# Kernel optimization log

Measured on AMD Instinct MI355X. Metric: run time of the kernel, lower is better.

Reference implementation:

```python
import jax, jax.numpy as jnp
import numpy as np

B, N, P, HID = 1024, 30, 16, 128
NR = N * (N - 1)          # 870 directed edges
DR, DE, DO, NT = 3, 5, 6, 5


def _lin(x, w, b):
    return x @ w.T + b


def setup_inputs() -> dict:
    key = jax.random.key(0)
    ks = jax.random.split(key, 24)

    def w(k, o, i):
        return jax.random.normal(k, (o, i), jnp.float32) * 0.05

    def bias(k, o):
        return jax.random.normal(k, (o,), jnp.float32) * 0.05

    return {
        "x": jax.random.normal(ks[0], (B, N, P), jnp.float32),
        "RR": jax.random.normal(ks[1], (B, N, NR), jnp.float32),
        "RS": jax.random.normal(ks[2], (B, N, NR), jnp.float32),
        "RA": jax.random.normal(ks[3], (B, DR, NR), jnp.float32),
        "fr1_w": w(ks[4], HID, 2 * P + DR), "fr1_b": bias(ks[5], HID),
        "fr2_w": w(ks[6], HID // 2, HID),   "fr2_b": bias(ks[7], HID // 2),
        "fr3_w": w(ks[8], DE, HID // 2),    "fr3_b": bias(ks[9], DE),
        "fo1_w": w(ks[10], HID, P + DE),    "fo1_b": bias(ks[11], HID),
        "fo2_w": w(ks[12], HID // 2, HID),  "fo2_b": bias(ks[13], HID // 2),
        "fo3_w": w(ks[14], DO, HID // 2),   "fo3_b": bias(ks[15], DO),
        "fc1_w": w(ks[16], HID, DO * N),    "fc1_b": bias(ks[17], HID),
        "fc2_w": w(ks[18], HID // 2, HID),  "fc2_b": bias(ks[19], HID // 2),
        "fc3_w": w(ks[20], NT, HID // 2),   "fc3_b": bias(ks[21], NT),
    }


def reference(x, RR, RS, RA,
              fr1_w, fr1_b, fr2_w, fr2_b, fr3_w, fr3_b,
              fo1_w, fo1_b, fo2_w, fo2_b, fo3_w, fo3_b,
              fc1_w, fc1_b, fc2_w, fc2_b, fc3_w, fc3_b):
    xt = jnp.swapaxes(x, 1, 2)                       # [B, P, N]
    Orr = jnp.einsum('bpn,bnr->bpr', xt, RR)          # [B, P, Nr]
    Ors = jnp.einsum('bpn,bnr->bpr', xt, RS)          # [B, P, Nr]
    Bm = jnp.concatenate([Orr, Ors, RA], axis=1)      # [B, 2P+Dr, Nr]
    Bm = jnp.swapaxes(Bm, 1, 2)                       # [B, Nr, 2P+Dr]
    h = jax.nn.relu(_lin(Bm, fr1_w, fr1_b))
    h = jax.nn.relu(_lin(h, fr2_w, fr2_b))
    E = jax.nn.relu(_lin(h, fr3_w, fr3_b))            # [B, Nr, De]
    Ebar = jnp.einsum('bre,bnr->ben', E, RR)          # E^T @ RR^T -> [B, De, N]
    C = jnp.concatenate([xt, Ebar], axis=1)           # [B, P+De, N]
    C = jnp.swapaxes(C, 1, 2)                         # [B, N, P+De]
    h = jax.nn.relu(_lin(C, fo1_w, fo1_b))
    h = jax.nn.relu(_lin(h, fo2_w, fo2_b))
    O = jax.nn.relu(_lin(h, fo3_w, fo3_b))            # [B, N, Do]
    f = O.reshape(O.shape[0], -1)                     # [B, Do*N]
    f = jax.nn.relu(_lin(f, fc1_w, fc1_b))
    f = jax.nn.relu(_lin(f, fc2_w, fc2_b))
    return _lin(f, fc3_w, fc3_b)                      # [B, n_targets]
```

## Files before the change

kernel.cpp:

```cpp
#include <hip/hip_runtime.h>

#define B_ 1024
#define N_ 30
#define P_ 16
#define NR_ 870
#define DR_ 3
#define DE_ 5
#define DO_ 6
#define NT_ 5

typedef unsigned short ushort_t;
typedef __attribute__((ext_vector_type(8))) short short8_t;
typedef __attribute__((ext_vector_type(4))) float f32x4;

union Frag { short8_t v; ushort_t u[8]; };

__device__ __forceinline__ float bf2f(ushort_t u) {
    union { unsigned int i; float f; } v; v.i = ((unsigned int)u) << 16; return v.f;
}
__device__ __forceinline__ ushort_t f2bf(float f) {
    union { float f; unsigned int i; } v; v.f = f;
    unsigned int x = v.i;
    return (ushort_t)((x + 0x7FFFu + ((x >> 16) & 1u)) >> 16);
}
__device__ __forceinline__ void split(float v, ushort_t& h, ushort_t& l) {
    h = f2bf(v);
    float r = v - bf2f(h);
    l = f2bf(r);
}
__device__ __forceinline__ f32x4 mfma(short8_t a, short8_t b, f32x4 c) {
    return __builtin_amdgcn_mfma_f32_16x16x32_bf16(a, b, c, 0, 0, 0);
}

__global__ __launch_bounds__(256) void k_prep(
    const float* __restrict__ x,  const float* __restrict__ w1,
    const float* __restrict__ w2, const float* __restrict__ wo1,
    const float* __restrict__ wo2,
    ushort_t* __restrict__ xAh,  ushort_t* __restrict__ xAl,
    ushort_t* __restrict__ w1h,  ushort_t* __restrict__ w1l,
    ushort_t* __restrict__ w2h,  ushort_t* __restrict__ w2l,
    ushort_t* __restrict__ wo1h, ushort_t* __restrict__ wo1l,
    ushort_t* __restrict__ wo2h, ushort_t* __restrict__ wo2l)
{
    const int blk = blockIdx.x, tid = threadIdx.x;
    if (blk < 1024) {
        int b = blk;
        for (int idx = tid; idx < 512; idx += 256) {
            int lane = idx >> 3, j = idx & 7;
            int p = lane & 15, n = (lane >> 4) * 8 + j;
            float v = (n < N_) ? x[(b * N_ + n) * P_ + p] : 0.f;
            ushort_t h_, l_; split(v, h_, l_);
            xAh[b * 512 + idx] = h_; xAl[b * 512 + idx] = l_;
        }
    } else if (blk == 1024) {
        for (int idx = tid; idx < 16 * 512; idx += 256) {
            int f = idx >> 9, eps = idx & 511;
            int lane = eps >> 3, j = eps & 7;
            int mt = f >> 1, kt = f & 1;
            int m = mt * 16 + (lane & 15);
            int k = kt * 32 + (lane >> 4) * 8 + j;
            float v = (k < 35) ? w1[m * 35 + k] : 0.f;
            ushort_t h_, l_; split(v, h_, l_);
            w1h[idx] = h_; w1l[idx] = l_;
        }
    } else if (blk == 1025) {
        for (int idx = tid; idx < 16 * 512; idx += 256) {
            int f = idx >> 9, eps = idx & 511;
            int lane = eps >> 3, j = eps & 7;
            int mt = f >> 2, kt = f & 3;
            int m = mt * 16 + (lane & 15);
            int k = kt * 32 + (lane >> 4) * 8 + j;
            float v = w2[m * 128 + k];
            ushort_t h_, l_; split(v, h_, l_);
            w2h[idx] = h_; w2l[idx] = l_;
        }
    } else if (blk == 1026) {
        for (int idx = tid; idx < 8 * 512; idx += 256) {
            int f = idx >> 9, eps = idx & 511;
            int lane = eps >> 3, j = eps & 7;
            int m = f * 16 + (lane & 15);
            int k = (lane >> 4) * 8 + j;
            float v = (k < 21) ? wo1[m * 21 + k] : 0.f;
            ushort_t h_, l_; split(v, h_, l_);
            wo1h[idx] = h_; wo1l[idx] = l_;
        }
    } else {
        for (int idx = tid; idx < 16 * 512; idx += 256) {
            int f = idx >> 9, eps = idx & 511;
            int lane = eps >> 3, j = eps & 7;
            int mt = f >> 2, kt = f & 3;
            int m = mt * 16 + (lane & 15);
            int k = kt * 32 + (lane >> 4) * 8 + j;
            float v = wo2[m * 128 + k];
            ushort_t h_, l_; split(v, h_, l_);
            wo2h[idx] = h_; wo2l[idx] = l_;
        }
    }
}

__global__ __launch_bounds__(256) void k_edge(
    const float* __restrict__ RR, const float* __restrict__ RS,
    const float* __restrict__ RA,
    const float* __restrict__ b1, const float* __restrict__ b2,
    const float* __restrict__ w3, const float* __restrict__ b3,
    const ushort_t* __restrict__ xAh, const ushort_t* __restrict__ xAl,
    const ushort_t* __restrict__ w1h, const ushort_t* __restrict__ w1l,
    const ushort_t* __restrict__ w2h, const ushort_t* __restrict__ w2l,
    float* __restrict__ Ebar)
{
    const int b   = blockIdx.y;
    const int r0  = blockIdx.x * 64;
    const int tid = threadIdx.x;
    const int lane = tid & 63;
    const int wv   = tid >> 6;
    const int l15  = lane & 15;
    const int q    = lane >> 4;

    __shared__ union {
        ushort_t aT[2][64][72];
        float    h2T[64][68];
    } u1;
    __shared__ union {
        ushort_t h1T[2][64][72];
        float    rs[30][70];
    } u2;
    __shared__ float rrs[30][70];
    __shared__ float Ee[64][6];
    __shared__ float b1s[128], b2s[64];

    if (tid < 128) b1s[tid] = b1[tid];
    if (tid < 64)  b2s[tid] = b2[tid];

    for (int idx = tid; idx < 30 * 32; idx += 256) {
        int n = idx >> 5, g = idx & 31;
        int r = r0 + 2 * g;
        const float* pr = &RR[(b * N_ + n) * NR_];
        const float* ps = &RS[(b * N_ + n) * NR_];
        float v0, v1, s0, s1;
        if (r + 1 < NR_) {
            float2 a = *(const float2*)&pr[r]; v0 = a.x; v1 = a.y;
            float2 c = *(const float2*)&ps[r]; s0 = c.x; s1 = c.y;
        } else {
            int ra_ = r < NR_ ? r : NR_ - 1;
            int rb_ = (r + 1) < NR_ ? (r + 1) : NR_ - 1;
            v0 = pr[ra_]; v1 = pr[rb_]; s0 = ps[ra_]; s1 = ps[rb_];
        }
        rrs[n][2 * g] = v0;  rrs[n][2 * g + 1] = v1;
        u2.rs[n][2 * g] = s0; u2.rs[n][2 * g + 1] = s1;
    }
    __syncthreads();

    const int eloc = wv * 16 + l15;
    const int r = r0 + eloc;
    const bool rvalid = (r < NR_);

    {
        Frag xh, xl;
        xh.v = ((const short8_t*)xAh)[b * 64 + lane];
        xl.v = ((const short8_t*)xAl)[b * 64 + lane];

        Frag rrh, rrl, rsh, rsl;
        #pragma unroll
        for (int j = 0; j < 8; ++j) {
            int n = q * 8 + j;
            float vr = 0.f, vs = 0.f;
            if (n < N_) { vr = rrs[n][eloc]; vs = u2.rs[n][eloc]; }
            ushort_t h_, l_;
            split(vr, h_, l_); rrh.u[j] = h_; rrl.u[j] = l_;
            split(vs, h_, l_); rsh.u[j] = h_; rsl.u[j] = l_;
        }

        f32x4 aR = {0.f,0.f,0.f,0.f}, aS = {0.f,0.f,0.f,0.f};
        aR = mfma(xh.v, rrh.v, aR); aR = mfma(xl.v, rrh.v, aR); aR = mfma(xh.v, rrl.v, aR);
        aS = mfma(xh.v, rsh.v, aS); aS = mfma(xl.v, rsh.v, aS); aS = mfma(xh.v, rsl.v, aS);

        uint4 z = {0u,0u,0u,0u};
        *(uint4*)&u1.aT[0][eloc][32 + q * 8] = z;
        *(uint4*)&u1.aT[1][eloc][32 + q * 8] = z;

        ushort4 ph, pl; ushort_t h_, l_;
        split(aR[0], h_, l_); ph.x = h_; pl.x = l_;
        split(aR[1], h_, l_); ph.y = h_; pl.y = l_;
        split(aR[2], h_, l_); ph.z = h_; pl.z = l_;
        split(aR[3], h_, l_); ph.w = h_; pl.w = l_;
        *(ushort4*)&u1.aT[0][eloc][q * 4] = ph;
        *(ushort4*)&u1.aT[1][eloc][q * 4] = pl;
        split(aS[0], h_, l_); ph.x = h_; pl.x = l_;
        split(aS[1], h_, l_); ph.y = h_; pl.y = l_;
        split(aS[2], h_, l_); ph.z = h_; pl.z = l_;
        split(aS[3], h_, l_); ph.w = h_; pl.w = l_;
        *(ushort4*)&u1.aT[0][eloc][16 + q * 4] = ph;
        *(ushort4*)&u1.aT[1][eloc][16 + q * 4] = pl;

        if (q < DR_) {
            float v = rvalid ? RA[(b * DR_ + q) * NR_ + r] : 0.f;
            split(v, h_, l_);
            u1.aT[0][eloc][32 + q] = h_;
            u1.aT[1][eloc][32 + q] = l_;
        }
    }
    __syncthreads();

    short8_t W2hf[4], W2lf[4];
    #pragma unroll
    for (int kt = 0; kt < 4; ++kt) {
        W2hf[kt] = ((const short8_t*)w2h)[(wv * 4 + kt) * 64 + lane];
        W2lf[kt] = ((const short8_t*)w2l)[(wv * 4 + kt) * 64 + lane];
    }
    f32x4 acc2[4];
    #pragma unroll
    for (int et = 0; et < 4; ++et) acc2[et] = (f32x4){0.f,0.f,0.f,0.f};

    #pragma unroll
    for (int hf = 0; hf < 2; ++hf) {
        {
            const int mt = hf * 4 + wv;
            short8_t W1hf_[2], W1lf_[2];
            #pragma unroll
            for (int kt = 0; kt < 2; ++kt) {
                W1hf_[kt] = ((const short8_t*)w1h)[(mt * 2 + kt) * 64 + lane];
                W1lf_[kt] = ((const short8_t*)w1l)[(mt * 2 + kt) * 64 + lane];
            }
            #pragma unroll
            for (int et = 0; et < 4; ++et) {
                int e = et * 16 + l15;
                f32x4 acc = {0.f,0.f,0.f,0.f};
                #pragma unroll
                for (int kt = 0; kt < 2; ++kt) {
                    short8_t Bh = *(const short8_t*)&u1.aT[0][e][kt * 32 + q * 8];
                    short8_t Bl = *(const short8_t*)&u1.aT[1][e][kt * 32 + q * 8];
                    acc = mfma(W1hf_[kt], Bh, acc);
                    acc = mfma(W1lf_[kt], Bh, acc);
                    acc = mfma(W1hf_[kt], Bl, acc);
                }
                ushort4 ph, pl; ushort_t h_, l_; float hv;
                hv = fmaxf(acc[0] + b1s[mt * 16 + q * 4 + 0], 0.f); split(hv, h_, l_); ph.x = h_; pl.x = l_;
                hv = fmaxf(acc[1] + b1s[mt * 16 + q * 4 + 1], 0.f); split(hv, h_, l_); ph.y = h_; pl.y = l_;
                hv = fmaxf(acc[2] + b1s[mt * 16 + q * 4 + 2], 0.f); split(hv, h_, l_); ph.z = h_; pl.z = l_;
                hv = fmaxf(acc[3] + b1s[mt * 16 + q * 4 + 3], 0.f); split(hv, h_, l_); ph.w = h_; pl.w = l_;
                *(ushort4*)&u2.h1T[0][e][wv * 16 + q * 4] = ph;
                *(ushort4*)&u2.h1T[1][e][wv * 16 + q * 4] = pl;
            }
        }
        __syncthreads();

        #pragma unroll
        for (int et = 0; et < 4; ++et) {
            int e = et * 16 + l15;
            #pragma unroll
            for (int ktl = 0; ktl < 2; ++ktl) {
                short8_t bh = *(const short8_t*)&u2.h1T[0][e][ktl * 32 + q * 8];
                short8_t bl = *(const short8_t*)&u2.h1T[1][e][ktl * 32 + q * 8];
                acc2[et] = mfma(W2hf[hf * 2 + ktl], bh, acc2[et]);
                acc2[et] = mfma(W2lf[hf * 2 + ktl], bh, acc2[et]);
                acc2[et] = mfma(W2hf[hf * 2 + ktl], bl, acc2[et]);
            }
        }
        if (hf == 1) {
            #pragma unroll
            for (int et = 0; et < 4; ++et) {
                int e = et * 16 + l15;
                float4 st;
                st.x = fmaxf(acc2[et][0] + b2s[wv * 16 + q * 4 + 0], 0.f);
                st.y = fmaxf(acc2[et][1] + b2s[wv * 16 + q * 4 + 1], 0.f);
                st.z = fmaxf(acc2[et][2] + b2s[wv * 16 + q * 4 + 2], 0.f);
                st.w = fmaxf(acc2[et][3] + b2s[wv * 16 + q * 4 + 3], 0.f);
                *(float4*)&u1.h2T[e][wv * 16 + q * 4] = st;
            }
        }
        __syncthreads();
    }

    for (int it = tid; it < 64 * DE_; it += 256) {
        int e = it / DE_, i = it - e * DE_;
        float s = b3[i];
        const float* wr = w3 + i * 64;
        #pragma unroll
        for (int k = 0; k < 64; k += 4) {
            float4 hv = *(const float4*)&u1.h2T[e][k];
            float4 wv4 = *(const float4*)&wr[k];
            s += hv.x * wv4.x + hv.y * wv4.y + hv.z * wv4.z + hv.w * wv4.w;
        }
        Ee[e][i] = ((r0 + e) < NR_) ? fmaxf(s, 0.f) : 0.f;
    }
    __syncthreads();

    if (tid < DE_ * N_) {
        int i = tid / N_, n = tid - i * N_;
        float s = 0.f;
        #pragma unroll
        for (int e = 0; e < 64; ++e) s += Ee[e][i] * rrs[n][e];
        atomicAdd(&Ebar[(b * DE_ + i) * N_ + n], s);
    }
}

__global__ __launch_bounds__(256) void k_node(
    const float* __restrict__ x, const float* __restrict__ Ebar,
    const float* __restrict__ bo1, const float* __restrict__ bo2,
    const float* __restrict__ wo3, const float* __restrict__ bo3,
    const ushort_t* __restrict__ wo1h, const ushort_t* __restrict__ wo1l,
    const ushort_t* __restrict__ wo2h, const ushort_t* __restrict__ wo2l,
    float* __restrict__ f180)
{
    const int b0 = blockIdx.x * 2;
    const int tid = threadIdx.x;
    const int lane = tid & 63;
    const int wv = tid >> 6;
    const int l15 = lane & 15;
    const int q = lane >> 4;

    __shared__ ushort_t cT[2][64][40];
    __shared__ ushort_t h1T[2][64][136];
    __shared__ float h2T[64][68];
    __shared__ float b1s[128], b2s[64];

    if (tid < 128) b1s[tid] = bo1[tid];
    if (tid < 64)  b2s[tid] = bo2[tid];

    for (int idx = tid; idx < 64 * 32; idx += 256) {
        int c = idx >> 5, k = idx & 31;
        int bb = c >> 5, n = c & 31;
        float v = 0.f;
        if (n < N_) {
            if (k < 16)      v = x[((b0 + bb) * N_ + n) * P_ + k];
            else if (k < 21) v = Ebar[((b0 + bb) * DE_ + (k - 16)) * N_ + n];
        }
        ushort_t h_, l_; split(v, h_, l_);
        cT[0][c][k] = h_; cT[1][c][k] = l_;
    }
    __syncthreads();

    {
        short8_t Wh[2], Wl[2];
        #pragma unroll
        for (int mi = 0; mi < 2; ++mi) {
            int mt = wv + mi * 4;
            Wh[mi] = ((const short8_t*)wo1h)[mt * 64 + lane];
            Wl[mi] = ((const short8_t*)wo1l)[mt * 64 + lane];
        }
        #pragma unroll
        for (int et = 0; et < 4; ++et) {
            int c = et * 16 + l15;
            short8_t bh = *(const short8_t*)&cT[0][c][q * 8];
            short8_t bl = *(const short8_t*)&cT[1][c][q * 8];
            #pragma unroll
            for (int mi = 0; mi < 2; ++mi) {
                int mt = wv + mi * 4;
                f32x4 acc = {0.f,0.f,0.f,0.f};
                acc = mfma(Wh[mi], bh, acc);
                acc = mfma(Wl[mi], bh, acc);
                acc = mfma(Wh[mi], bl, acc);
                ushort4 ph, pl; ushort_t h_, l_; float hv;
                hv = fmaxf(acc[0] + b1s[mt * 16 + q * 4 + 0], 0.f); split(hv, h_, l_); ph.x = h_; pl.x = l_;
                hv = fmaxf(acc[1] + b1s[mt * 16 + q * 4 + 1], 0.f); split(hv, h_, l_); ph.y = h_; pl.y = l_;
                hv = fmaxf(acc[2] + b1s[mt * 16 + q * 4 + 2], 0.f); split(hv, h_, l_); ph.z = h_; pl.z = l_;
                hv = fmaxf(acc[3] + b1s[mt * 16 + q * 4 + 3], 0.f); split(hv, h_, l_); ph.w = h_; pl.w = l_;
                *(ushort4*)&h1T[0][c][mt * 16 + q * 4] = ph;
                *(ushort4*)&h1T[1][c][mt * 16 + q * 4] = pl;
            }
        }
    }
    __syncthreads();

    {
        short8_t Wh[4], Wl[4];
        #pragma unroll
        for (int kt = 0; kt < 4; ++kt) {
            Wh[kt] = ((const short8_t*)wo2h)[(wv * 4 + kt) * 64 + lane];
            Wl[kt] = ((const short8_t*)wo2l)[(wv * 4 + kt) * 64 + lane];
        }
        #pragma unroll
        for (int et = 0; et < 4; ++et) {
            int c = et * 16 + l15;
            f32x4 acc = {0.f,0.f,0.f,0.f};
            #pragma unroll
            for (int kt = 0; kt < 4; ++kt) {
                short8_t bh = *(const short8_t*)&h1T[0][c][kt * 32 + q * 8];
                short8_t bl = *(const short8_t*)&h1T[1][c][kt * 32 + q * 8];
                acc = mfma(Wh[kt], bh, acc);
                acc = mfma(Wl[kt], bh, acc);
                acc = mfma(Wh[kt], bl, acc);
            }
            float4 st;
            st.x = fmaxf(acc[0] + b2s[wv * 16 + q * 4 + 0], 0.f);
            st.y = fmaxf(acc[1] + b2s[wv * 16 + q * 4 + 1], 0.f);
            st.z = fmaxf(acc[2] + b2s[wv * 16 + q * 4 + 2], 0.f);
            st.w = fmaxf(acc[3] + b2s[wv * 16 + q * 4 + 3], 0.f);
            *(float4*)&h2T[c][wv * 16 + q * 4] = st;
        }
    }
    __syncthreads();

    for (int it = tid; it < 384; it += 256) {
        int c = it / DO_, i = it - c * DO_;
        if (c < 64) {
            int bb = c >> 5, n = c & 31;
            if (n < N_) {
                float s = bo3[i];
                const float* wr = wo3 + i * 64;
                #pragma unroll
                for (int k = 0; k < 64; k += 4) {
                    float4 hv = *(const float4*)&h2T[c][k];
                    float4 wv4 = *(const float4*)&wr[k];
                    s += hv.x * wv4.x + hv.y * wv4.y + hv.z * wv4.z + hv.w * wv4.w;
                }
                f180[(b0 + bb) * 180 + n * DO_ + i] = fmaxf(s, 0.f);
            }
        }
    }
}

__global__ __launch_bounds__(256) void k_final(
    const float* __restrict__ f180,
    const float* __restrict__ wc1, const float* __restrict__ bc1,
    const float* __restrict__ wc2, const float* __restrict__ bc2,
    const float* __restrict__ wc3, const float* __restrict__ bc3,
    float* __restrict__ out)
{
    const int b0 = blockIdx.x * 2, tid = threadIdx.x;
    __shared__ float fs[2][184];
    __shared__ float h1s[2][128];
    __shared__ float h2s[2][64];

    for (int i = tid; i < 2 * 180; i += 256)
        fs[i / 180][i % 180] = f180[(b0 + i / 180) * 180 + (i % 180)];
    __syncthreads();

    {
        int bl = tid >> 7, j = tid & 127;
        const float* wr = wc1 + j * 180;
        float s = bc1[j];
        #pragma unroll 5
        for (int k = 0; k < 180; k += 4) {
            float4 wv = *(const float4*)&wr[k];
            s += fs[bl][k] * wv.x + fs[bl][k + 1] * wv.y
               + fs[bl][k + 2] * wv.z + fs[bl][k + 3] * wv.w;
        }
        h1s[bl][j] = fmaxf(s, 0.f);
    }
    __syncthreads();

    if (tid < 128) {
        int bl = tid >> 6, j = tid & 63;
        const float* wr = wc2 + j * 128;
        float s = bc2[j];
        #pragma unroll 4
        for (int k = 0; k < 128; k += 4) {
            float4 wv = *(const float4*)&wr[k];
            s += h1s[bl][k] * wv.x + h1s[bl][k + 1] * wv.y
               + h1s[bl][k + 2] * wv.z + h1s[bl][k + 3] * wv.w;
        }
        h2s[bl][j] = fmaxf(s, 0.f);
    }
    __syncthreads();

    if (tid < 10) {
        int bl = tid / 5, t = tid - bl * 5;
        const float* wr = wc3 + t * 64;
        float s = bc3[t];
        #pragma unroll
        for (int k = 0; k < 64; k += 4) {
            float4 wv = *(const float4*)&wr[k];
            s += h2s[bl][k] * wv.x + h2s[bl][k + 1] * wv.y
               + h2s[bl][k + 2] * wv.z + h2s[bl][k + 3] * wv.w;
        }
        out[(b0 + bl) * NT_ + t] = s;
    }
}

extern "C" void kernel_launch(void* const* d_in, const int* in_sizes, int n_in,
                              void* d_out, int out_size, void* d_ws, size_t ws_size,
                              hipStream_t stream)
{
    const float* x    = (const float*)d_in[0];
    const float* RR   = (const float*)d_in[1];
    const float* RS   = (const float*)d_in[2];
    const float* RA   = (const float*)d_in[3];
    const float* fr1w = (const float*)d_in[4];
    const float* fr1b = (const float*)d_in[5];
    const float* fr2w = (const float*)d_in[6];
    const float* fr2b = (const float*)d_in[7];
    const float* fr3w = (const float*)d_in[8];
    const float* fr3b = (const float*)d_in[9];
    const float* fo1w = (const float*)d_in[10];
    const float* fo1b = (const float*)d_in[11];
    const float* fo2w = (const float*)d_in[12];
    const float* fo2b = (const float*)d_in[13];
    const float* fo3w = (const float*)d_in[14];
    const float* fo3b = (const float*)d_in[15];
    const float* fc1w = (const float*)d_in[16];
    const float* fc1b = (const float*)d_in[17];
    const float* fc2w = (const float*)d_in[18];
    const float* fc2b = (const float*)d_in[19];
    const float* fc3w = (const float*)d_in[20];
    const float* fc3b = (const float*)d_in[21];
    float* out = (float*)d_out;

    float* Ebar = (float*)d_ws;
    float* f180 = Ebar + B_ * DE_ * N_;
    ushort_t* base = (ushort_t*)(f180 + B_ * 180);
    ushort_t* xAh  = base;             ushort_t* xAl  = xAh  + 1024 * 512;
    ushort_t* w1h  = xAl  + 1024*512;  ushort_t* w1l  = w1h  + 16 * 512;
    ushort_t* w2h  = w1l  + 16*512;    ushort_t* w2l  = w2h  + 16 * 512;
    ushort_t* wo1h = w2l  + 16*512;    ushort_t* wo1l = wo1h + 8 * 512;
    ushort_t* wo2h = wo1l + 8*512;     ushort_t* wo2l = wo2h + 16 * 512;

    hipMemsetAsync(Ebar, 0, (size_t)B_ * DE_ * N_ * sizeof(float), stream);

    k_prep<<<1028, 256, 0, stream>>>(x, fr1w, fr2w, fo1w, fo2w,
                                     xAh, xAl, w1h, w1l, w2h, w2l,
                                     wo1h, wo1l, wo2h, wo2l);

    dim3 g1(14, B_);
    k_edge<<<g1, 256, 0, stream>>>(RR, RS, RA, fr1b, fr2b, fr3w, fr3b,
                                   xAh, xAl, w1h, w1l, w2h, w2l, Ebar);
    k_node<<<B_ / 2, 256, 0, stream>>>(x, Ebar, fo1b, fo2b, fo3w, fo3b,
                                       wo1h, wo1l, wo2h, wo2l, f180);
    k_final<<<B_ / 2, 256, 0, stream>>>(f180, fc1w, fc1b, fc2w, fc2b,
                                        fc3w, fc3b, out);
}
```

Measured before the change: 632.0 us.

## Fuse node and final MLPs, load RR/RS directly, use packed bf16 conversion

```diff
diff --git a/kernel.cpp b/kernel.cpp
--- a/kernel.cpp
+++ b/kernel.cpp
@@ -13,7 +13,7 @@
 typedef __attribute__((ext_vector_type(8))) short short8_t;
 typedef __attribute__((ext_vector_type(4))) float f32x4;
 
-union Frag { short8_t v; ushort_t u[8]; };
+union Frag { short8_t v; ushort_t u[8]; unsigned int d[4]; };
 
 __device__ __forceinline__ float bf2f(ushort_t u) {
     union { unsigned int i; float f; } v; v.i = ((unsigned int)u) << 16; return v.f;
@@ -27,6 +27,18 @@
     h = f2bf(v);
     float r = v - bf2f(h);
     l = f2bf(r);
+}
+__device__ __forceinline__ unsigned int cvtpk(float a, float b) {
+    unsigned int r;
+    asm("v_cvt_pk_bf16_f32 %0, %1, %2" : "=v"(r) : "v"(a), "v"(b));
+    return r;
+}
+__device__ __forceinline__ void split2(float a, float b,
+                                       unsigned int& h, unsigned int& l) {
+    h = cvtpk(a, b);
+    union { unsigned int i; float f; } x0, x1;
+    x0.i = h << 16; x1.i = h & 0xFFFF0000u;
+    l = cvtpk(a - x0.f, b - x1.f);
 }
 __device__ __forceinline__ f32x4 mfma(short8_t a, short8_t b, f32x4 c) {
     return __builtin_amdgcn_mfma_f32_16x16x32_bf16(a, b, c, 0, 0, 0);
@@ -120,54 +132,35 @@
         ushort_t aT[2][64][72];
         float    h2T[64][68];
     } u1;
-    __shared__ union {
-        ushort_t h1T[2][64][72];
-        float    rs[30][70];
-    } u2;
-    __shared__ float rrs[30][70];
+    __shared__ ushort_t h1T[2][64][72];
     __shared__ float Ee[64][6];
     __shared__ float b1s[128], b2s[64];
 
     if (tid < 128) b1s[tid] = b1[tid];
     if (tid < 64)  b2s[tid] = b2[tid];
-
-    for (int idx = tid; idx < 30 * 32; idx += 256) {
-        int n = idx >> 5, g = idx & 31;
-        int r = r0 + 2 * g;
-        const float* pr = &RR[(b * N_ + n) * NR_];
-        const float* ps = &RS[(b * N_ + n) * NR_];
-        float v0, v1, s0, s1;
-        if (r + 1 < NR_) {
-            float2 a = *(const float2*)&pr[r]; v0 = a.x; v1 = a.y;
-            float2 c = *(const float2*)&ps[r]; s0 = c.x; s1 = c.y;
-        } else {
-            int ra_ = r < NR_ ? r : NR_ - 1;
-            int rb_ = (r + 1) < NR_ ? (r + 1) : NR_ - 1;
-            v0 = pr[ra_]; v1 = pr[rb_]; s0 = ps[ra_]; s1 = ps[rb_];
-        }
-        rrs[n][2 * g] = v0;  rrs[n][2 * g + 1] = v1;
-        u2.rs[n][2 * g] = s0; u2.rs[n][2 * g + 1] = s1;
-    }
-    __syncthreads();
 
     const int eloc = wv * 16 + l15;
     const int r = r0 + eloc;
     const bool rvalid = (r < NR_);
+    const int rc = rvalid ? r : NR_ - 1;
 
     {
         Frag xh, xl;
         xh.v = ((const short8_t*)xAh)[b * 64 + lane];
         xl.v = ((const short8_t*)xAl)[b * 64 + lane];
 
-        Frag rrh, rrl, rsh, rsl;
+        float vr[8], vs[8];
         #pragma unroll
         for (int j = 0; j < 8; ++j) {
             int n = q * 8 + j;
-            float vr = 0.f, vs = 0.f;
-            if (n < N_) { vr = rrs[n][eloc]; vs = u2.rs[n][eloc]; }
-            ushort_t h_, l_;
-            split(vr, h_, l_); rrh.u[j] = h_; rrl.u[j] = l_;
-            split(vs, h_, l_); rsh.u[j] = h_; rsl.u[j] = l_;
+            vr[j] = (n < N_) ? RR[(b * N_ + n) * NR_ + rc] : 0.f;
+            vs[j] = (n < N_) ? RS[(b * N_ + n) * NR_ + rc] : 0.f;
+        }
+        Frag rrh, rrl, rsh, rsl;
+        #pragma unroll
+        for (int d0 = 0; d0 < 4; ++d0) {
+            split2(vr[2*d0], vr[2*d0+1], rrh.d[d0], rrl.d[d0]);
+            split2(vs[2*d0], vs[2*d0+1], rsh.d[d0], rsl.d[d0]);
         }
 
         f32x4 aR = {0.f,0.f,0.f,0.f}, aS = {0.f,0.f,0.f,0.f};
@@ -178,23 +171,19 @@
         *(uint4*)&u1.aT[0][eloc][32 + q * 8] = z;
         *(uint4*)&u1.aT[1][eloc][32 + q * 8] = z;
 
-        ushort4 ph, pl; ushort_t h_, l_;
-        split(aR[0], h_, l_); ph.x = h_; pl.x = l_;
-        split(aR[1], h_, l_); ph.y = h_; pl.y = l_;
-        split(aR[2], h_, l_); ph.z = h_; pl.z = l_;
-        split(aR[3], h_, l_); ph.w = h_; pl.w = l_;
-        *(ushort4*)&u1.aT[0][eloc][q * 4] = ph;
-        *(ushort4*)&u1.aT[1][eloc][q * 4] = pl;
-        split(aS[0], h_, l_); ph.x = h_; pl.x = l_;
-        split(aS[1], h_, l_); ph.y = h_; pl.y = l_;
-        split(aS[2], h_, l_); ph.z = h_; pl.z = l_;
-        split(aS[3], h_, l_); ph.w = h_; pl.w = l_;
-        *(ushort4*)&u1.aT[0][eloc][16 + q * 4] = ph;
-        *(ushort4*)&u1.aT[1][eloc][16 + q * 4] = pl;
+        unsigned int h01, h23, l01, l23;
+        split2(aR[0], aR[1], h01, l01); split2(aR[2], aR[3], h23, l23);
+        { uint2 hh = {h01, h23}, ll = {l01, l23};
+          *(uint2*)&u1.aT[0][eloc][q * 4] = hh;
+          *(uint2*)&u1.aT[1][eloc][q * 4] = ll; }
+        split2(aS[0], aS[1], h01, l01); split2(aS[2], aS[3], h23, l23);
+        { uint2 hh = {h01, h23}, ll = {l01, l23};
+          *(uint2*)&u1.aT[0][eloc][16 + q * 4] = hh;
+          *(uint2*)&u1.aT[1][eloc][16 + q * 4] = ll; }
 
         if (q < DR_) {
             float v = rvalid ? RA[(b * DR_ + q) * NR_ + r] : 0.f;
-            split(v, h_, l_);
+            ushort_t h_, l_; split(v, h_, l_);
             u1.aT[0][eloc][32 + q] = h_;
             u1.aT[1][eloc][32 + q] = l_;
         }
@@ -233,13 +222,15 @@
                     acc = mfma(W1lf_[kt], Bh, acc);
                     acc = mfma(W1hf_[kt], Bl, acc);
                 }
-                ushort4 ph, pl; ushort_t h_, l_; float hv;
-                hv = fmaxf(acc[0] + b1s[mt * 16 + q * 4 + 0], 0.f); split(hv, h_, l_); ph.x = h_; pl.x = l_;
-                hv = fmaxf(acc[1] + b1s[mt * 16 + q * 4 + 1], 0.f); split(hv, h_, l_); ph.y = h_; pl.y = l_;
-                hv = fmaxf(acc[2] + b1s[mt * 16 + q * 4 + 2], 0.f); split(hv, h_, l_); ph.z = h_; pl.z = l_;
-                hv = fmaxf(acc[3] + b1s[mt * 16 + q * 4 + 3], 0.f); split(hv, h_, l_); ph.w = h_; pl.w = l_;
-                *(ushort4*)&u2.h1T[0][e][wv * 16 + q * 4] = ph;
-                *(ushort4*)&u2.h1T[1][e][wv * 16 + q * 4] = pl;
+                float hv0 = fmaxf(acc[0] + b1s[mt * 16 + q * 4 + 0], 0.f);
+                float hv1 = fmaxf(acc[1] + b1s[mt * 16 + q * 4 + 1], 0.f);
+                float hv2 = fmaxf(acc[2] + b1s[mt * 16 + q * 4 + 2], 0.f);
+                float hv3 = fmaxf(acc[3] + b1s[mt * 16 + q * 4 + 3], 0.f);
+                unsigned int d01, d23, e01, e23;
+                split2(hv0, hv1, d01, e01); split2(hv2, hv3, d23, e23);
+                uint2 hh = {d01, d23}, ll = {e01, e23};
+                *(uint2*)&h1T[0][e][wv * 16 + q * 4] = hh;
+                *(uint2*)&h1T[1][e][wv * 16 + q * 4] = ll;
             }
         }
         __syncthreads();
@@ -249,8 +240,8 @@
             int e = et * 16 + l15;
             #pragma unroll
             for (int ktl = 0; ktl < 2; ++ktl) {
-                short8_t bh = *(const short8_t*)&u2.h1T[0][e][ktl * 32 + q * 8];
-                short8_t bl = *(const short8_t*)&u2.h1T[1][e][ktl * 32 + q * 8];
+                short8_t bh = *(const short8_t*)&h1T[0][e][ktl * 32 + q * 8];
+                short8_t bl = *(const short8_t*)&h1T[1][e][ktl * 32 + q * 8];
                 acc2[et] = mfma(W2hf[hf * 2 + ktl], bh, acc2[et]);
                 acc2[et] = mfma(W2lf[hf * 2 + ktl], bh, acc2[et]);
                 acc2[et] = mfma(W2hf[hf * 2 + ktl], bl, acc2[et]);
@@ -287,20 +278,24 @@
 
     if (tid < DE_ * N_) {
         int i = tid / N_, n = tid - i * N_;
+        const float* pr = &RR[(b * N_ + n) * NR_ + r0];
+        const int emax = (NR_ - r0 < 64) ? (NR_ - r0) : 64;
         float s = 0.f;
-        #pragma unroll
-        for (int e = 0; e < 64; ++e) s += Ee[e][i] * rrs[n][e];
+        for (int e = 0; e < emax; ++e) s += Ee[e][i] * pr[e];
         atomicAdd(&Ebar[(b * DE_ + i) * N_ + n], s);
     }
 }
 
-__global__ __launch_bounds__(256) void k_node(
+__global__ __launch_bounds__(256) void k_nodef(
     const float* __restrict__ x, const float* __restrict__ Ebar,
     const float* __restrict__ bo1, const float* __restrict__ bo2,
     const float* __restrict__ wo3, const float* __restrict__ bo3,
     const ushort_t* __restrict__ wo1h, const ushort_t* __restrict__ wo1l,
     const ushort_t* __restrict__ wo2h, const ushort_t* __restrict__ wo2l,
-    float* __restrict__ f180)
+    const float* __restrict__ wc1, const float* __restrict__ bc1,
+    const float* __restrict__ wc2, const float* __restrict__ bc2,
+    const float* __restrict__ wc3, const float* __restrict__ bc3,
+    float* __restrict__ out)
 {
     const int b0 = blockIdx.x * 2;
     const int tid = threadIdx.x;
@@ -309,7 +304,10 @@
     const int l15 = lane & 15;
     const int q = lane >> 4;
 
-    __shared__ ushort_t cT[2][64][40];
+    __shared__ union {
+        ushort_t cT[2][64][40];
+        struct { float fs[2][184]; float h1s[2][128]; float h2s[2][64]; } f;
+    } u2n;
     __shared__ ushort_t h1T[2][64][136];
     __shared__ float h2T[64][68];
     __shared__ float b1s[128], b2s[64];
@@ -326,7 +324,7 @@
             else if (k < 21) v = Ebar[((b0 + bb) * DE_ + (k - 16)) * N_ + n];
         }
         ushort_t h_, l_; split(v, h_, l_);
-        cT[0][c][k] = h_; cT[1][c][k] = l_;
+        u2n.cT[0][c][k] = h_; u2n.cT[1][c][k] = l_;
     }
     __syncthreads();
 
@@ -341,8 +339,8 @@
         #pragma unroll
         for (int et = 0; et < 4; ++et) {
             int c = et * 16 + l15;
-            short8_t bh = *(const short8_t*)&cT[0][c][q * 8];
-            short8_t bl = *(const short8_t*)&cT[1][c][q * 8];
+            short8_t bh = *(const short8_t*)&u2n.cT[0][c][q * 8];
+            short8_t bl = *(const short8_t*)&u2n.cT[1][c][q * 8];
             #pragma unroll
             for (int mi = 0; mi < 2; ++mi) {
                 int mt = wv + mi * 4;
@@ -350,13 +348,15 @@
                 acc = mfma(Wh[mi], bh, acc);
                 acc = mfma(Wl[mi], bh, acc);
                 acc = mfma(Wh[mi], bl, acc);
-                ushort4 ph, pl; ushort_t h_, l_; float hv;
-                hv = fmaxf(acc[0] + b1s[mt * 16 + q * 4 + 0], 0.f); split(hv, h_, l_); ph.x = h_; pl.x = l_;
-                hv = fmaxf(acc[1] + b1s[mt * 16 + q * 4 + 1], 0.f); split(hv, h_, l_); ph.y = h_; pl.y = l_;
-                hv = fmaxf(acc[2] + b1s[mt * 16 + q * 4 + 2], 0.f); split(hv, h_, l_); ph.z = h_; pl.z = l_;
-                hv = fmaxf(acc[3] + b1s[mt * 16 + q * 4 + 3], 0.f); split(hv, h_, l_); ph.w = h_; pl.w = l_;
-                *(ushort4*)&h1T[0][c][mt * 16 + q * 4] = ph;
-                *(ushort4*)&h1T[1][c][mt * 16 + q * 4] = pl;
+                float hv0 = fmaxf(acc[0] + b1s[mt * 16 + q * 4 + 0], 0.f);
+                float hv1 = fmaxf(acc[1] + b1s[mt * 16 + q * 4 + 1], 0.f);
+                float hv2 = fmaxf(acc[2] + b1s[mt * 16 + q * 4 + 2], 0.f);
+                float hv3 = fmaxf(acc[3] + b1s[mt * 16 + q * 4 + 3], 0.f);
+                unsigned int d01, d23, e01, e23;
+                split2(hv0, hv1, d01, e01); split2(hv2, hv3, d23, e23);
+                uint2 hh = {d01, d23}, ll = {e01, e23};
+                *(uint2*)&h1T[0][c][mt * 16 + q * 4] = hh;
+                *(uint2*)&h1T[1][c][mt * 16 + q * 4] = ll;
             }
         }
     }
@@ -404,26 +404,10 @@
                     float4 wv4 = *(const float4*)&wr[k];
                     s += hv.x * wv4.x + hv.y * wv4.y + hv.z * wv4.z + hv.w * wv4.w;
                 }
-                f180[(b0 + bb) * 180 + n * DO_ + i] = fmaxf(s, 0.f);
-            }
-        }
-    }
-}
-
-__global__ __launch_bounds__(256) void k_final(
-    const float* __restrict__ f180,
-    const float* __restrict__ wc1, const float* __restrict__ bc1,
-    const float* __restrict__ wc2, const float* __restrict__ bc2,
-    const float* __restrict__ wc3, const float* __restrict__ bc3,
-    float* __restrict__ out)
-{
-    const int b0 = blockIdx.x * 2, tid = threadIdx.x;
-    __shared__ float fs[2][184];
-    __shared__ float h1s[2][128];
-    __shared__ float h2s[2][64];
-
-    for (int i = tid; i < 2 * 180; i += 256)
-        fs[i / 180][i % 180] = f180[(b0 + i / 180) * 180 + (i % 180)];
+                u2n.f.fs[bb][n * DO_ + i] = fmaxf(s, 0.f);
+            }
+        }
+    }
     __syncthreads();
 
     {
@@ -432,11 +416,11 @@
         float s = bc1[j];
         #pragma unroll 5
         for (int k = 0; k < 180; k += 4) {
-            float4 wv = *(const float4*)&wr[k];
-            s += fs[bl][k] * wv.x + fs[bl][k + 1] * wv.y
-               + fs[bl][k + 2] * wv.z + fs[bl][k + 3] * wv.w;
-        }
-        h1s[bl][j] = fmaxf(s, 0.f);
+            float4 wv4 = *(const float4*)&wr[k];
+            s += u2n.f.fs[bl][k] * wv4.x + u2n.f.fs[bl][k + 1] * wv4.y
+               + u2n.f.fs[bl][k + 2] * wv4.z + u2n.f.fs[bl][k + 3] * wv4.w;
+        }
+        u2n.f.h1s[bl][j] = fmaxf(s, 0.f);
     }
     __syncthreads();
 
@@ -446,11 +430,11 @@
         float s = bc2[j];
         #pragma unroll 4
         for (int k = 0; k < 128; k += 4) {
-            float4 wv = *(const float4*)&wr[k];
-            s += h1s[bl][k] * wv.x + h1s[bl][k + 1] * wv.y
-               + h1s[bl][k + 2] * wv.z + h1s[bl][k + 3] * wv.w;
-        }
-        h2s[bl][j] = fmaxf(s, 0.f);
+            float4 wv4 = *(const float4*)&wr[k];
+            s += u2n.f.h1s[bl][k] * wv4.x + u2n.f.h1s[bl][k + 1] * wv4.y
+               + u2n.f.h1s[bl][k + 2] * wv4.z + u2n.f.h1s[bl][k + 3] * wv4.w;
+        }
+        u2n.f.h2s[bl][j] = fmaxf(s, 0.f);
     }
     __syncthreads();
 
@@ -460,9 +444,9 @@
         float s = bc3[t];
         #pragma unroll
         for (int k = 0; k < 64; k += 4) {
-            float4 wv = *(const float4*)&wr[k];
-            s += h2s[bl][k] * wv.x + h2s[bl][k + 1] * wv.y
-               + h2s[bl][k + 2] * wv.z + h2s[bl][k + 3] * wv.w;
+            float4 wv4 = *(const float4*)&wr[k];
+            s += u2n.f.h2s[bl][k] * wv4.x + u2n.f.h2s[bl][k + 1] * wv4.y
+               + u2n.f.h2s[bl][k + 2] * wv4.z + u2n.f.h2s[bl][k + 3] * wv4.w;
         }
         out[(b0 + bl) * NT_ + t] = s;
     }
@@ -497,8 +481,7 @@
     float* out = (float*)d_out;
 
     float* Ebar = (float*)d_ws;
-    float* f180 = Ebar + B_ * DE_ * N_;
-    ushort_t* base = (ushort_t*)(f180 + B_ * 180);
+    ushort_t* base = (ushort_t*)(Ebar + B_ * DE_ * N_);
     ushort_t* xAh  = base;             ushort_t* xAl  = xAh  + 1024 * 512;
     ushort_t* w1h  = xAl  + 1024*512;  ushort_t* w1l  = w1h  + 16 * 512;
     ushort_t* w2h  = w1l  + 16*512;    ushort_t* w2l  = w2h  + 16 * 512;
@@ -514,8 +497,7 @@
     dim3 g1(14, B_);
     k_edge<<<g1, 256, 0, stream>>>(RR, RS, RA, fr1b, fr2b, fr3w, fr3b,
                                    xAh, xAl, w1h, w1l, w2h, w2l, Ebar);
-    k_node<<<B_ / 2, 256, 0, stream>>>(x, Ebar, fo1b, fo2b, fo3w, fo3b,
-                                       wo1h, wo1l, wo2h, wo2l, f180);
-    k_final<<<B_ / 2, 256, 0, stream>>>(f180, fc1w, fc1b, fc2w, fc2b,
-                                        fc3w, fc3b, out);
-}
+    k_nodef<<<B_ / 2, 256, 0, stream>>>(x, Ebar, fo1b, fo2b, fo3w, fo3b,
+                                        wo1h, wo1l, wo2h, wo2l,
+                                        fc1w, fc1b, fc2w, fc2b, fc3w, fc3b, out);
+}
```

After: 549.9 us. -13.0%, faster.
